# Kernel optimization log

Measured on AMD Instinct MI355X. Metric: run time of the kernel, lower is better.

## Reference

```python
import jax, jax.numpy as jnp
import numpy as np

B, N = 4, 2048

def setup_inputs() -> dict:
    key = jax.random.key(0)
    k1, k2, k3, k4 = jax.random.split(key, 4)
    return {
        "xyz": jax.random.normal(k1, (B, N, 3), dtype=jnp.float32),
        "scales": jax.random.uniform(k2, (B, N, 3), dtype=jnp.float32),
        "rotations": jax.random.normal(k3, (B, N, 4), dtype=jnp.float32),
        "velocities": jax.random.normal(k4, (B, N, 3), dtype=jnp.float32),
    }

def _quat_to_rotmat(q):
    # q: (B, N, 4) -> (B, N, 3, 3), same formula as the torch module (no normalization)
    qw, qx, qy, qz = q[..., 0], q[..., 1], q[..., 2], q[..., 3]
    R = jnp.stack([
        1 - 2 * qy**2 - 2 * qz**2, 2 * qx * qy - 2 * qz * qw, 2 * qx * qz + 2 * qy * qw,
        2 * qx * qy + 2 * qz * qw, 1 - 2 * qx**2 - 2 * qz**2, 2 * qy * qz - 2 * qx * qw,
        2 * qx * qz - 2 * qy * qw, 2 * qy * qz + 2 * qx * qw, 1 - 2 * qx**2 - 2 * qy**2,
    ], axis=-1)
    return R.reshape(q.shape[0], q.shape[1], 3, 3)

def reference(xyz, scales, rotations, velocities):
    b, n, _ = xyz.shape
    diff = xyz[:, :, None, :] - xyz[:, None, :, :]          # (B,N,N,3)
    dist = jnp.sqrt(jnp.sum(diff * diff, axis=-1) + 1e-8)    # (B,N,N)
    direction = diff / dist[..., None]                        # (B,N,N,3)

    R = _quat_to_rotmat(rotations)                            # (B,N,3,3)
    u_R = jnp.einsum('bnmi,bnij->bnmj', direction, R)         # (B,N,N,3)
    u_R_S = u_R * scales[:, None, :, :]                       # scale of gaussian m
    r_directional = jnp.sqrt(jnp.sum(u_R_S * u_R_S, axis=-1))  # (B,N,N)
    r_total = r_directional + jnp.swapaxes(r_directional, 1, 2)

    overlap = jax.nn.relu(r_total - dist)                     # (B,N,N)
    spectral_repulsion = overlap**2 / (1 + 0.1 * overlap)

    v_rel = velocities[:, :, None, :] - velocities[:, None, :, :]
    v_approach = jnp.sum(v_rel * direction, axis=-1)          # (B,N,N)
    mskd_loss = jnp.sum(overlap * jax.nn.relu(-v_approach)) / (b * n * n)

    mask = jnp.eye(n, dtype=bool)[None]                       # zero self-pairs
    spectral_repulsion = jnp.where(mask, 0.0, spectral_repulsion)
    return jnp.mean(spectral_repulsion) + 0.1 * mskd_loss
```

## Files before the change

kernel.cpp:

```cpp
#include <hip/hip_runtime.h>

#define BB 4
#define NN 2048
#define NPTS (BB * NN)
#define TILE 512
#define TT (NN / TILE)
#define NTP (TT * (TT + 1) / 2)
#define MS 32
#define MSPL (TILE / MS)
#define JPB (NTP * MSPL)
#define NJOBS (JPB * BB)
#define BLK 256
#define ROWS 2
#define SCALE (2.0f / ((float)BB * (float)NN * (float)NN))

#define WS_COUNTER_OFF 0
#define WS_PART_OFF    256
#define WS_PACK_OFF    (1 << 20)
#define WS_NEEDED      (WS_PACK_OFF + (size_t)NPTS * 5 * 16)

__device__ __forceinline__ void quat_to_R(float qw, float qx, float qy, float qz, float* R) {
    R[0] = 1.f - 2.f * (qy * qy + qz * qz);
    R[1] = 2.f * (qx * qy - qz * qw);
    R[2] = 2.f * (qx * qz + qy * qw);
    R[3] = 2.f * (qx * qy + qz * qw);
    R[4] = 1.f - 2.f * (qx * qx + qz * qz);
    R[5] = 2.f * (qy * qz - qx * qw);
    R[6] = 2.f * (qx * qz - qy * qw);
    R[7] = 2.f * (qy * qz + qx * qw);
    R[8] = 1.f - 2.f * (qx * qx + qy * qy);
}

__global__ __launch_bounds__(256) void pack_kernel(
    const float* __restrict__ xyz, const float* __restrict__ scales,
    const float* __restrict__ rot, const float* __restrict__ vel,
    float4* __restrict__ pk)
{
    const int i = blockIdx.x * 256 + threadIdx.x;
    if (i >= NPTS) return;
    const size_t i3 = 3 * (size_t)i;
    const float4 q = *reinterpret_cast<const float4*>(rot + 4 * (size_t)i);
    float R[9];
    quat_to_R(q.x, q.y, q.z, q.w, R);
    pk[0 * NPTS + i] = make_float4(xyz[i3], xyz[i3 + 1], xyz[i3 + 2], scales[i3]);
    pk[1 * NPTS + i] = make_float4(scales[i3 + 1], scales[i3 + 2], vel[i3], vel[i3 + 1]);
    pk[2 * NPTS + i] = make_float4(vel[i3 + 2], R[0], R[1], R[2]);
    pk[3 * NPTS + i] = make_float4(R[3], R[4], R[5], R[6]);
    pk[4 * NPTS + i] = make_float4(R[7], R[8], 0.f, 0.f);
}

__global__ __launch_bounds__(BLK) void pair_kernel(
    const float4* __restrict__ pk,
    float* __restrict__ partials, unsigned int* __restrict__ counter,
    float* __restrict__ outp)
{
    __shared__ float4 sm[MS][5];
    __shared__ float wsum[4];
    __shared__ int lastflag;

    const int tid = threadIdx.x;
    const int jid = blockIdx.x;
    const int b   = jid / JPB;
    const int rem = jid % JPB;
    const int p   = rem / MSPL;
    const int sl  = rem % MSPL;

    int ti = 0;
    while ((ti + 1) * (ti + 2) / 2 <= p) ++ti;
    const int tj = p - ti * (ti + 1) / 2;
    const bool diag = (ti == tj);

    const int n0 = ti * TILE;
    const int m0 = tj * TILE + sl * MS;
    const int gb = b * NN;

    if (tid < MS) {
        const int gi = gb + m0 + tid;
        sm[tid][0] = pk[0 * NPTS + gi];
        sm[tid][1] = pk[1 * NPTS + gi];
        sm[tid][2] = pk[2 * NPTS + gi];
        sm[tid][3] = pk[3 * NPTS + gi];
        sm[tid][4] = pk[4 * NPTS + gi];
    }

    float px[ROWS], py[ROWS], pz[ROWS];
    float sx[ROWS], sy[ROWS], sz[ROWS];
    float vx[ROWS], vy[ROWS], vz[ROWS];
    float Rn[ROWS][9];
    int   nidx[ROWS];
    #pragma unroll
    for (int r = 0; r < ROWS; ++r) {
        const int n  = n0 + tid + 256 * r;
        nidx[r] = n;
        const int gi = gb + n;
        const float4 n0v = pk[0 * NPTS + gi];
        const float4 n1v = pk[1 * NPTS + gi];
        const float4 n2v = pk[2 * NPTS + gi];
        const float4 n3v = pk[3 * NPTS + gi];
        const float4 n4v = pk[4 * NPTS + gi];
        px[r] = n0v.x; py[r] = n0v.y; pz[r] = n0v.z;
        sx[r] = n0v.w; sy[r] = n1v.x; sz[r] = n1v.y;
        vx[r] = n1v.z; vy[r] = n1v.w; vz[r] = n2v.x;
        Rn[r][0] = n2v.y; Rn[r][1] = n2v.z; Rn[r][2] = n2v.w;
        Rn[r][3] = n3v.x; Rn[r][4] = n3v.y; Rn[r][5] = n3v.z;
        Rn[r][6] = n3v.w; Rn[r][7] = n4v.x; Rn[r][8] = n4v.y;
    }

    __syncthreads();

    float acc = 0.f;

    auto inner = [&](bool isDiag) {
        #pragma unroll 4
        for (int j = 0; j < MS; ++j) {
            const int m = m0 + j;
            const float4 c0 = sm[j][0];
            const float4 c1 = sm[j][1];
            const float4 c2 = sm[j][2];
            const float4 c3 = sm[j][3];
            const float4 c4 = sm[j][4];
            #pragma unroll
            for (int r = 0; r < ROWS; ++r) {
                const float dx = px[r] - c0.x, dy = py[r] - c0.y, dz = pz[r] - c0.z;
                const float d2 = fmaf(dx, dx, fmaf(dy, dy, fmaf(dz, dz, 1e-8f)));
                const float rinv = __builtin_amdgcn_rsqf(d2);
                const float a0 = fmaf(dx, Rn[r][0], fmaf(dy, Rn[r][3], dz * Rn[r][6])) * c0.w;
                const float a1 = fmaf(dx, Rn[r][1], fmaf(dy, Rn[r][4], dz * Rn[r][7])) * c1.x;
                const float a2 = fmaf(dx, Rn[r][2], fmaf(dy, Rn[r][5], dz * Rn[r][8])) * c1.y;
                const float qa = __builtin_amdgcn_sqrtf(fmaf(a0, a0, fmaf(a1, a1, a2 * a2)));
                const float b0 = fmaf(dx, c2.y, fmaf(dy, c3.x, dz * c3.w)) * sx[r];
                const float b1 = fmaf(dx, c2.z, fmaf(dy, c3.y, dz * c4.x)) * sy[r];
                const float b2 = fmaf(dx, c2.w, fmaf(dy, c3.z, dz * c4.y)) * sz[r];
                const float qb = __builtin_amdgcn_sqrtf(fmaf(b0, b0, fmaf(b1, b1, b2 * b2)));
                const float ww = fmaxf(qa + qb - d2, 0.f);
                const float ov = ww * rinv;
                const float rc = __builtin_amdgcn_rcpf(fmaf(0.1f, ov, 1.f));
                const float vdot = fmaf(vx[r] - c1.z, dx,
                                   fmaf(vy[r] - c1.w, dy, (vz[r] - c2.x) * dz));
                const float ramp = fmaxf(-vdot * rinv, 0.f);
                float t = ov * fmaf(ov, rc, 0.1f * ramp);
                if (isDiag && !(m < nidx[r])) t = 0.f;
                acc += t;
            }
        }
    };
    if (diag) inner(true); else inner(false);

    #pragma unroll
    for (int off = 32; off > 0; off >>= 1)
        acc += __shfl_down(acc, off, 64);
    if ((tid & 63) == 0) wsum[tid >> 6] = acc;
    __syncthreads();

    if (tid == 0) {
        partials[jid] = wsum[0] + wsum[1] + wsum[2] + wsum[3];
        __threadfence();
        const unsigned int done = atomicAdd(counter, 1u);
        lastflag = (done == (unsigned int)(NJOBS - 1));
    }
    __syncthreads();

    if (lastflag) {
        __threadfence();
        const float4* p4 = reinterpret_cast<const float4*>(partials);
        float s = 0.f;
        for (int i = tid; i < NJOBS / 4; i += BLK) {
            const float4 v = p4[i];
            s += v.x + v.y + v.z + v.w;
        }
        #pragma unroll
        for (int off = 32; off > 0; off >>= 1)
            s += __shfl_down(s, off, 64);
        if ((tid & 63) == 0) wsum[tid >> 6] = s;
        __syncthreads();
        if (tid == 0) outp[0] = (wsum[0] + wsum[1] + wsum[2] + wsum[3]) * SCALE;
    }
}

__global__ __launch_bounds__(256) void naive_kernel(
    const float* __restrict__ xyz, const float* __restrict__ scales,
    const float* __restrict__ rot, const float* __restrict__ vel,
    float* __restrict__ outp)
{
    const int g = blockIdx.x * 256 + threadIdx.x;
    const int b = g / NN, n = g % NN;
    const size_t i3 = ((size_t)b * NN + n) * 3;
    const float4 qn = *reinterpret_cast<const float4*>(rot + ((size_t)b * NN + n) * 4);
    float Rn[9];
    quat_to_R(qn.x, qn.y, qn.z, qn.w, Rn);
    const float px = xyz[i3], py = xyz[i3+1], pz = xyz[i3+2];
    const float sx = scales[i3], sy = scales[i3+1], sz = scales[i3+2];
    const float vx = vel[i3], vy = vel[i3+1], vz = vel[i3+2];
    float acc = 0.f;
    for (int m = 0; m < n; ++m) {
        const size_t j3 = ((size_t)b * NN + m) * 3;
        const float4 qm = *reinterpret_cast<const float4*>(rot + ((size_t)b * NN + m) * 4);
        float Rm[9];
        quat_to_R(qm.x, qm.y, qm.z, qm.w, Rm);
        const float dx = px - xyz[j3], dy = py - xyz[j3+1], dz = pz - xyz[j3+2];
        const float d2 = fmaf(dx, dx, fmaf(dy, dy, fmaf(dz, dz, 1e-8f)));
        const float rinv = __builtin_amdgcn_rsqf(d2);
        const float a0 = fmaf(dx, Rn[0], fmaf(dy, Rn[3], dz*Rn[6])) * scales[j3];
        const float a1 = fmaf(dx, Rn[1], fmaf(dy, Rn[4], dz*Rn[7])) * scales[j3+1];
        const float a2 = fmaf(dx, Rn[2], fmaf(dy, Rn[5], dz*Rn[8])) * scales[j3+2];
        const float qa = __builtin_amdgcn_sqrtf(fmaf(a0,a0,fmaf(a1,a1,a2*a2)));
        const float b0 = fmaf(dx, Rm[0], fmaf(dy, Rm[3], dz*Rm[6])) * sx;
        const float b1 = fmaf(dx, Rm[1], fmaf(dy, Rm[4], dz*Rm[7])) * sy;
        const float b2 = fmaf(dx, Rm[2], fmaf(dy, Rm[5], dz*Rm[8])) * sz;
        const float qb = __builtin_amdgcn_sqrtf(fmaf(b0,b0,fmaf(b1,b1,b2*b2)));
        const float ww = fmaxf(qa + qb - d2, 0.f);
        const float ov = ww * rinv;
        const float rc = __builtin_amdgcn_rcpf(fmaf(0.1f, ov, 1.f));
        const float vdot = fmaf(vx - vel[j3], dx, fmaf(vy - vel[j3+1], dy, (vz - vel[j3+2]) * dz));
        const float ramp = fmaxf(-vdot * rinv, 0.f);
        acc += ov * fmaf(ov, rc, 0.1f * ramp);
    }
    #pragma unroll
    for (int off = 32; off > 0; off >>= 1)
        acc += __shfl_down(acc, off, 64);
    if ((threadIdx.x & 63) == 0) atomicAdd(outp, acc * SCALE);
}

extern "C" void kernel_launch(void* const* d_in, const int* in_sizes, int n_in,
                              void* d_out, int out_size, void* d_ws, size_t ws_size,
                              hipStream_t stream)
{
    const float* xyz    = (const float*)d_in[0];
    const float* scales = (const float*)d_in[1];
    const float* rot    = (const float*)d_in[2];
    const float* vel    = (const float*)d_in[3];
    float* out = (float*)d_out;

    if (ws_size >= WS_NEEDED) {
        unsigned int* counter = (unsigned int*)((char*)d_ws + WS_COUNTER_OFF);
        float* partials       = (float*)((char*)d_ws + WS_PART_OFF);
        float4* pk            = (float4*)((char*)d_ws + WS_PACK_OFF);
        hipMemsetAsync(counter, 0, sizeof(unsigned int), stream);
        pack_kernel<<<(NPTS + 255) / 256, 256, 0, stream>>>(xyz, scales, rot, vel, pk);
        pair_kernel<<<NJOBS, BLK, 0, stream>>>(pk, partials, counter, out);
    } else {
        hipMemsetAsync(d_out, 0, sizeof(float), stream);
        naive_kernel<<<NPTS / 256, 256, 0, stream>>>(xyz, scales, rot, vel, out);
    }
}
```

Before: 37.85 us.

## Retile pair kernel to 128-row tiles with float2 packed math across warps

Shrinks the row tile from 512 to 128 and gives each warp its own 16-column slice of a 64-column chunk, while every lane handles two rows at once. The per-pair arithmetic is written with float2 vectors so the compiler can emit packed FP32 FMA/mul instructions. This produces many more, smaller blocks, which improves load balance over the triangular tile set, and the packed math cuts the number of issued VALU instructions. In exchange there are more partials to reduce and more per-block setup and staging loads per pair computed.

```diff
diff --git a/kernel.cpp b/kernel.cpp
--- a/kernel.cpp
+++ b/kernel.cpp
@@ -3,21 +3,26 @@
 #define BB 4
 #define NN 2048
 #define NPTS (BB * NN)
-#define TILE 512
-#define TT (NN / TILE)
+#define TS 128
+#define TT (NN / TS)
 #define NTP (TT * (TT + 1) / 2)
-#define MS 32
-#define MSPL (TILE / MS)
+#define MC 64
+#define MSPL (TS / MC)
+#define MPW (MC / 4)
 #define JPB (NTP * MSPL)
 #define NJOBS (JPB * BB)
 #define BLK 256
-#define ROWS 2
 #define SCALE (2.0f / ((float)BB * (float)NN * (float)NN))
 
 #define WS_COUNTER_OFF 0
 #define WS_PART_OFF    256
 #define WS_PACK_OFF    (1 << 20)
 #define WS_NEEDED      (WS_PACK_OFF + (size_t)NPTS * 5 * 16)
+
+typedef float f2 __attribute__((ext_vector_type(2)));
+
+__device__ __forceinline__ f2 ffma(f2 a, f2 b, f2 c) { return __builtin_elementwise_fma(a, b, c); }
+__device__ __forceinline__ f2 fmax2(f2 a, f2 b)      { return __builtin_elementwise_max(a, b); }
 
 __device__ __forceinline__ void quat_to_R(float qw, float qx, float qy, float qz, float* R) {
     R[0] = 1.f - 2.f * (qy * qy + qz * qz);
@@ -54,45 +59,45 @@
     float* __restrict__ partials, unsigned int* __restrict__ counter,
     float* __restrict__ outp)
 {
-    __shared__ float4 sm[MS][5];
+    __shared__ float4 sm[MC][5];
     __shared__ float wsum[4];
     __shared__ int lastflag;
 
-    const int tid = threadIdx.x;
-    const int jid = blockIdx.x;
-    const int b   = jid / JPB;
-    const int rem = jid % JPB;
-    const int p   = rem / MSPL;
-    const int sl  = rem % MSPL;
+    const int tid  = threadIdx.x;
+    const int lane = tid & 63;
+    const int w    = tid >> 6;
+    const int jid  = blockIdx.x;
+    const int b    = jid / JPB;
+    const int rem  = jid % JPB;
+    const int p    = rem / MSPL;
+    const int mcch = rem % MSPL;
 
     int ti = 0;
     while ((ti + 1) * (ti + 2) / 2 <= p) ++ti;
     const int tj = p - ti * (ti + 1) / 2;
     const bool diag = (ti == tj);
 
-    const int n0 = ti * TILE;
-    const int m0 = tj * TILE + sl * MS;
-    const int gb = b * NN;
-
-    if (tid < MS) {
-        const int gi = gb + m0 + tid;
-        sm[tid][0] = pk[0 * NPTS + gi];
-        sm[tid][1] = pk[1 * NPTS + gi];
-        sm[tid][2] = pk[2 * NPTS + gi];
-        sm[tid][3] = pk[3 * NPTS + gi];
-        sm[tid][4] = pk[4 * NPTS + gi];
-    }
-
-    float px[ROWS], py[ROWS], pz[ROWS];
-    float sx[ROWS], sy[ROWS], sz[ROWS];
-    float vx[ROWS], vy[ROWS], vz[ROWS];
-    float Rn[ROWS][9];
-    int   nidx[ROWS];
+    const int n_base = ti * TS;
+    const int m_blk  = tj * TS + mcch * MC;
+    const int gb     = b * NN;
+
+    {
+        int idx = tid;
+        #pragma unroll 2
+        for (int itr = 0; itr < 2 && idx < MC * 5; ++itr, idx += 256) {
+            const int c = idx >> 6;
+            const int j = idx & 63;
+            sm[j][c] = pk[c * NPTS + gb + m_blk + j];
+        }
+    }
+
+    const int nx = n_base + lane;
+    const int ny = nx + 64;
+    f2 px, py, pz, sx, sy, sz, vx, vy, vz;
+    f2 Rn[9];
     #pragma unroll
-    for (int r = 0; r < ROWS; ++r) {
-        const int n  = n0 + tid + 256 * r;
-        nidx[r] = n;
-        const int gi = gb + n;
+    for (int r = 0; r < 2; ++r) {
+        const int gi = gb + (r == 0 ? nx : ny);
         const float4 n0v = pk[0 * NPTS + gi];
         const float4 n1v = pk[1 * NPTS + gi];
         const float4 n2v = pk[2 * NPTS + gi];
@@ -101,55 +106,77 @@
         px[r] = n0v.x; py[r] = n0v.y; pz[r] = n0v.z;
         sx[r] = n0v.w; sy[r] = n1v.x; sz[r] = n1v.y;
         vx[r] = n1v.z; vy[r] = n1v.w; vz[r] = n2v.x;
-        Rn[r][0] = n2v.y; Rn[r][1] = n2v.z; Rn[r][2] = n2v.w;
-        Rn[r][3] = n3v.x; Rn[r][4] = n3v.y; Rn[r][5] = n3v.z;
-        Rn[r][6] = n3v.w; Rn[r][7] = n4v.x; Rn[r][8] = n4v.y;
+        Rn[0][r] = n2v.y; Rn[1][r] = n2v.z; Rn[2][r] = n2v.w;
+        Rn[3][r] = n3v.x; Rn[4][r] = n3v.y; Rn[5][r] = n3v.z;
+        Rn[6][r] = n3v.w; Rn[7][r] = n4v.x; Rn[8][r] = n4v.y;
     }
 
     __syncthreads();
 
-    float acc = 0.f;
+    f2 acc = (f2)(0.f);
+    const int jb = w * MPW;
 
     auto inner = [&](bool isDiag) {
         #pragma unroll 4
-        for (int j = 0; j < MS; ++j) {
-            const int m = m0 + j;
+        for (int jj = 0; jj < MPW; ++jj) {
+            const int j = jb + jj;
+            const int m = m_blk + j;
             const float4 c0 = sm[j][0];
             const float4 c1 = sm[j][1];
             const float4 c2 = sm[j][2];
             const float4 c3 = sm[j][3];
             const float4 c4 = sm[j][4];
-            #pragma unroll
-            for (int r = 0; r < ROWS; ++r) {
-                const float dx = px[r] - c0.x, dy = py[r] - c0.y, dz = pz[r] - c0.z;
-                const float d2 = fmaf(dx, dx, fmaf(dy, dy, fmaf(dz, dz, 1e-8f)));
-                const float rinv = __builtin_amdgcn_rsqf(d2);
-                const float a0 = fmaf(dx, Rn[r][0], fmaf(dy, Rn[r][3], dz * Rn[r][6])) * c0.w;
-                const float a1 = fmaf(dx, Rn[r][1], fmaf(dy, Rn[r][4], dz * Rn[r][7])) * c1.x;
-                const float a2 = fmaf(dx, Rn[r][2], fmaf(dy, Rn[r][5], dz * Rn[r][8])) * c1.y;
-                const float qa = __builtin_amdgcn_sqrtf(fmaf(a0, a0, fmaf(a1, a1, a2 * a2)));
-                const float b0 = fmaf(dx, c2.y, fmaf(dy, c3.x, dz * c3.w)) * sx[r];
-                const float b1 = fmaf(dx, c2.z, fmaf(dy, c3.y, dz * c4.x)) * sy[r];
-                const float b2 = fmaf(dx, c2.w, fmaf(dy, c3.z, dz * c4.y)) * sz[r];
-                const float qb = __builtin_amdgcn_sqrtf(fmaf(b0, b0, fmaf(b1, b1, b2 * b2)));
-                const float ww = fmaxf(qa + qb - d2, 0.f);
-                const float ov = ww * rinv;
-                const float rc = __builtin_amdgcn_rcpf(fmaf(0.1f, ov, 1.f));
-                const float vdot = fmaf(vx[r] - c1.z, dx,
-                                   fmaf(vy[r] - c1.w, dy, (vz[r] - c2.x) * dz));
-                const float ramp = fmaxf(-vdot * rinv, 0.f);
-                float t = ov * fmaf(ov, rc, 0.1f * ramp);
-                if (isDiag && !(m < nidx[r])) t = 0.f;
-                acc += t;
+
+            const f2 dx = px - c0.x, dy = py - c0.y, dz = pz - c0.z;
+            f2 d2 = ffma(dz, dz, (f2)(1e-8f));
+            d2 = ffma(dy, dy, d2);
+            d2 = ffma(dx, dx, d2);
+            f2 rinv;
+            rinv[0] = __builtin_amdgcn_rsqf(d2[0]);
+            rinv[1] = __builtin_amdgcn_rsqf(d2[1]);
+
+            const f2 a0 = ffma(dx, Rn[0], ffma(dy, Rn[3], dz * Rn[6])) * c0.w;
+            const f2 a1 = ffma(dx, Rn[1], ffma(dy, Rn[4], dz * Rn[7])) * c1.x;
+            const f2 a2 = ffma(dx, Rn[2], ffma(dy, Rn[5], dz * Rn[8])) * c1.y;
+            const f2 qa2 = ffma(a0, a0, ffma(a1, a1, a2 * a2));
+            f2 qa;
+            qa[0] = __builtin_amdgcn_sqrtf(qa2[0]);
+            qa[1] = __builtin_amdgcn_sqrtf(qa2[1]);
+
+            const f2 b0 = ffma(dx, (f2)(c2.y), ffma(dy, (f2)(c3.x), dz * c3.w)) * sx;
+            const f2 b1 = ffma(dx, (f2)(c2.z), ffma(dy, (f2)(c3.y), dz * c4.x)) * sy;
+            const f2 b2 = ffma(dx, (f2)(c2.w), ffma(dy, (f2)(c3.z), dz * c4.y)) * sz;
+            const f2 qb2 = ffma(b0, b0, ffma(b1, b1, b2 * b2));
+            f2 qb;
+            qb[0] = __builtin_amdgcn_sqrtf(qb2[0]);
+            qb[1] = __builtin_amdgcn_sqrtf(qb2[1]);
+
+            const f2 ww = fmax2(qa + qb - d2, (f2)(0.f));
+            const f2 ov = ww * rinv;
+            const f2 den = ffma(ov, (f2)(0.1f), (f2)(1.f));
+            f2 rc;
+            rc[0] = __builtin_amdgcn_rcpf(den[0]);
+            rc[1] = __builtin_amdgcn_rcpf(den[1]);
+
+            const f2 vdot = ffma(vx - c1.z, dx, ffma(vy - c1.w, dy, (vz - c2.x) * dz));
+            const f2 ramp = fmax2(-vdot * rinv, (f2)(0.f));
+
+            f2 t = ov * ffma(ov, rc, ramp * 0.1f);
+            if (isDiag) {
+                t[0] = (m < nx) ? t[0] : 0.f;
+                t[1] = (m < ny) ? t[1] : 0.f;
             }
+            acc += t;
         }
     };
     if (diag) inner(true); else inner(false);
 
+    float a = acc[0] + acc[1];
+
     #pragma unroll
     for (int off = 32; off > 0; off >>= 1)
-        acc += __shfl_down(acc, off, 64);
-    if ((tid & 63) == 0) wsum[tid >> 6] = acc;
+        a += __shfl_down(a, off, 64);
+    if (lane == 0) wsum[w] = a;
     __syncthreads();
 
     if (tid == 0) {
@@ -171,7 +198,7 @@
         #pragma unroll
         for (int off = 32; off > 0; off >>= 1)
             s += __shfl_down(s, off, 64);
-        if ((tid & 63) == 0) wsum[tid >> 6] = s;
+        if (lane == 0) wsum[w] = s;
         __syncthreads();
         if (tid == 0) outp[0] = (wsum[0] + wsum[1] + wsum[2] + wsum[3]) * SCALE;
     }
```

Measured after the change: 38.77 us. 2.4% more time.

## Retile pair kernel into 256-row groups with 64-column strips to trim diagonal waste

Applied to the files above, without the earlier changes.

Replaces the 512x512 triangular tile pairs (each split into 32-column slices, two rows per thread) with 256-row groups. Each group is paired only with the 64-column strips up to and including its diagonal, giving 144 jobs per batch. This is meant to cut the redundant work on diagonal tiles, which were fully computed and then masked, and it drops the tile-index search loop. Each thread now handles one row, so there is less instruction-level parallelism per thread and fewer blocks are launched. Shared memory moves to a component-major layout and is filled cooperatively by all threads.

```diff
diff --git a/kernel.cpp b/kernel.cpp
--- a/kernel.cpp
+++ b/kernel.cpp
@@ -3,15 +3,12 @@
 #define BB 4
 #define NN 2048
 #define NPTS (BB * NN)
-#define TILE 512
-#define TT (NN / TILE)
-#define NTP (TT * (TT + 1) / 2)
-#define MS 32
-#define MSPL (TILE / MS)
-#define JPB (NTP * MSPL)
+#define RGR 256
+#define NG (NN / RGR)
+#define MW 64
+#define JPB 144
 #define NJOBS (JPB * BB)
 #define BLK 256
-#define ROWS 2
 #define SCALE (2.0f / ((float)BB * (float)NN * (float)NN))
 
 #define WS_COUNTER_OFF 0
@@ -54,97 +51,77 @@
     float* __restrict__ partials, unsigned int* __restrict__ counter,
     float* __restrict__ outp)
 {
-    __shared__ float4 sm[MS][5];
+    __shared__ float4 sm[5][MW];
     __shared__ float wsum[4];
     __shared__ int lastflag;
 
     const int tid = threadIdx.x;
     const int jid = blockIdx.x;
     const int b   = jid / JPB;
-    const int rem = jid % JPB;
-    const int p   = rem / MSPL;
-    const int sl  = rem % MSPL;
-
-    int ti = 0;
-    while ((ti + 1) * (ti + 2) / 2 <= p) ++ti;
-    const int tj = p - ti * (ti + 1) / 2;
-    const bool diag = (ti == tj);
-
-    const int n0 = ti * TILE;
-    const int m0 = tj * TILE + sl * MS;
+    const int r   = jid % JPB;
+
+    int g = 0;
+    #pragma unroll
+    for (int gg = 1; gg < NG; ++gg)
+        if (r >= 2 * gg * (gg + 1)) g = gg;
+    const int s  = r - 2 * g * (g + 1);
+    const int m0 = s * MW;
+    const int n  = g * RGR + tid;
     const int gb = b * NN;
 
-    if (tid < MS) {
-        const int gi = gb + m0 + tid;
-        sm[tid][0] = pk[0 * NPTS + gi];
-        sm[tid][1] = pk[1 * NPTS + gi];
-        sm[tid][2] = pk[2 * NPTS + gi];
-        sm[tid][3] = pk[3 * NPTS + gi];
-        sm[tid][4] = pk[4 * NPTS + gi];
-    }
-
-    float px[ROWS], py[ROWS], pz[ROWS];
-    float sx[ROWS], sy[ROWS], sz[ROWS];
-    float vx[ROWS], vy[ROWS], vz[ROWS];
-    float Rn[ROWS][9];
-    int   nidx[ROWS];
-    #pragma unroll
-    for (int r = 0; r < ROWS; ++r) {
-        const int n  = n0 + tid + 256 * r;
-        nidx[r] = n;
-        const int gi = gb + n;
-        const float4 n0v = pk[0 * NPTS + gi];
-        const float4 n1v = pk[1 * NPTS + gi];
-        const float4 n2v = pk[2 * NPTS + gi];
-        const float4 n3v = pk[3 * NPTS + gi];
-        const float4 n4v = pk[4 * NPTS + gi];
-        px[r] = n0v.x; py[r] = n0v.y; pz[r] = n0v.z;
-        sx[r] = n0v.w; sy[r] = n1v.x; sz[r] = n1v.y;
-        vx[r] = n1v.z; vy[r] = n1v.w; vz[r] = n2v.x;
-        Rn[r][0] = n2v.y; Rn[r][1] = n2v.z; Rn[r][2] = n2v.w;
-        Rn[r][3] = n3v.x; Rn[r][4] = n3v.y; Rn[r][5] = n3v.z;
-        Rn[r][6] = n3v.w; Rn[r][7] = n4v.x; Rn[r][8] = n4v.y;
-    }
+    {
+        int e = tid;
+        #pragma unroll 2
+        for (int it = 0; it < 2 && e < 5 * MW; ++it, e += BLK) {
+            const int c  = e >> 6;
+            const int pt = e & 63;
+            sm[c][pt] = pk[c * NPTS + gb + m0 + pt];
+        }
+    }
+
+    const int gi = gb + n;
+    const float4 n0v = pk[0 * NPTS + gi];
+    const float4 n1v = pk[1 * NPTS + gi];
+    const float4 n2v = pk[2 * NPTS + gi];
+    const float4 n3v = pk[3 * NPTS + gi];
+    const float4 n4v = pk[4 * NPTS + gi];
+    const float px = n0v.x, py = n0v.y, pz = n0v.z;
+    const float sx = n0v.w, sy = n1v.x, sz = n1v.y;
+    const float vx = n1v.z, vy = n1v.w, vz = n2v.x;
+    const float Rn0 = n2v.y, Rn1 = n2v.z, Rn2 = n2v.w;
+    const float Rn3 = n3v.x, Rn4 = n3v.y, Rn5 = n3v.z;
+    const float Rn6 = n3v.w, Rn7 = n4v.x, Rn8 = n4v.y;
 
     __syncthreads();
 
     float acc = 0.f;
 
-    auto inner = [&](bool isDiag) {
-        #pragma unroll 4
-        for (int j = 0; j < MS; ++j) {
-            const int m = m0 + j;
-            const float4 c0 = sm[j][0];
-            const float4 c1 = sm[j][1];
-            const float4 c2 = sm[j][2];
-            const float4 c3 = sm[j][3];
-            const float4 c4 = sm[j][4];
-            #pragma unroll
-            for (int r = 0; r < ROWS; ++r) {
-                const float dx = px[r] - c0.x, dy = py[r] - c0.y, dz = pz[r] - c0.z;
-                const float d2 = fmaf(dx, dx, fmaf(dy, dy, fmaf(dz, dz, 1e-8f)));
-                const float rinv = __builtin_amdgcn_rsqf(d2);
-                const float a0 = fmaf(dx, Rn[r][0], fmaf(dy, Rn[r][3], dz * Rn[r][6])) * c0.w;
-                const float a1 = fmaf(dx, Rn[r][1], fmaf(dy, Rn[r][4], dz * Rn[r][7])) * c1.x;
-                const float a2 = fmaf(dx, Rn[r][2], fmaf(dy, Rn[r][5], dz * Rn[r][8])) * c1.y;
-                const float qa = __builtin_amdgcn_sqrtf(fmaf(a0, a0, fmaf(a1, a1, a2 * a2)));
-                const float b0 = fmaf(dx, c2.y, fmaf(dy, c3.x, dz * c3.w)) * sx[r];
-                const float b1 = fmaf(dx, c2.z, fmaf(dy, c3.y, dz * c4.x)) * sy[r];
-                const float b2 = fmaf(dx, c2.w, fmaf(dy, c3.z, dz * c4.y)) * sz[r];
-                const float qb = __builtin_amdgcn_sqrtf(fmaf(b0, b0, fmaf(b1, b1, b2 * b2)));
-                const float ww = fmaxf(qa + qb - d2, 0.f);
-                const float ov = ww * rinv;
-                const float rc = __builtin_amdgcn_rcpf(fmaf(0.1f, ov, 1.f));
-                const float vdot = fmaf(vx[r] - c1.z, dx,
-                                   fmaf(vy[r] - c1.w, dy, (vz[r] - c2.x) * dz));
-                const float ramp = fmaxf(-vdot * rinv, 0.f);
-                float t = ov * fmaf(ov, rc, 0.1f * ramp);
-                if (isDiag && !(m < nidx[r])) t = 0.f;
-                acc += t;
-            }
-        }
-    };
-    if (diag) inner(true); else inner(false);
+    #pragma unroll 4
+    for (int j = 0; j < MW; ++j) {
+        const float4 c0 = sm[0][j];
+        const float4 c1 = sm[1][j];
+        const float4 c2 = sm[2][j];
+        const float4 c3 = sm[3][j];
+        const float4 c4 = sm[4][j];
+        const float dx = px - c0.x, dy = py - c0.y, dz = pz - c0.z;
+        const float d2 = fmaf(dx, dx, fmaf(dy, dy, fmaf(dz, dz, 1e-8f)));
+        const float rinv = __builtin_amdgcn_rsqf(d2);
+        const float a0 = fmaf(dx, Rn0, fmaf(dy, Rn3, dz * Rn6)) * c0.w;
+        const float a1 = fmaf(dx, Rn1, fmaf(dy, Rn4, dz * Rn7)) * c1.x;
+        const float a2 = fmaf(dx, Rn2, fmaf(dy, Rn5, dz * Rn8)) * c1.y;
+        const float qa = __builtin_amdgcn_sqrtf(fmaf(a0, a0, fmaf(a1, a1, a2 * a2)));
+        const float b0 = fmaf(dx, c2.y, fmaf(dy, c3.x, dz * c3.w)) * sx;
+        const float b1 = fmaf(dx, c2.z, fmaf(dy, c3.y, dz * c4.x)) * sy;
+        const float b2 = fmaf(dx, c2.w, fmaf(dy, c3.z, dz * c4.y)) * sz;
+        const float qb = __builtin_amdgcn_sqrtf(fmaf(b0, b0, fmaf(b1, b1, b2 * b2)));
+        const float ww = fmaxf(qa + qb - d2, 0.f);
+        const float ov = ww * rinv;
+        const float rc = __builtin_amdgcn_rcpf(fmaf(0.1f, ov, 1.f));
+        const float vdot = fmaf(vx - c1.z, dx, fmaf(vy - c1.w, dy, (vz - c2.x) * dz));
+        const float ramp = fmaxf(-vdot * rinv, 0.f);
+        const float t = ov * fmaf(ov, rc, 0.1f * ramp);
+        acc += (m0 + j < n) ? t : 0.f;
+    }
 
     #pragma unroll
     for (int off = 32; off > 0; off >>= 1)
@@ -163,15 +140,15 @@
     if (lastflag) {
         __threadfence();
         const float4* p4 = reinterpret_cast<const float4*>(partials);
-        float s = 0.f;
+        float s2 = 0.f;
         for (int i = tid; i < NJOBS / 4; i += BLK) {
             const float4 v = p4[i];
-            s += v.x + v.y + v.z + v.w;
+            s2 += v.x + v.y + v.z + v.w;
         }
         #pragma unroll
         for (int off = 32; off > 0; off >>= 1)
-            s += __shfl_down(s, off, 64);
-        if ((tid & 63) == 0) wsum[tid >> 6] = s;
+            s2 += __shfl_down(s2, off, 64);
+        if ((tid & 63) == 0) wsum[tid >> 6] = s2;
         __syncthreads();
         if (tid == 0) outp[0] = (wsum[0] + wsum[1] + wsum[2] + wsum[3]) * SCALE;
     }
@@ -182,8 +159,8 @@
     const float* __restrict__ rot, const float* __restrict__ vel,
     float* __restrict__ outp)
 {
-    const int g = blockIdx.x * 256 + threadIdx.x;
-    const int b = g / NN, n = g % NN;
+    const int gth = blockIdx.x * 256 + threadIdx.x;
+    const int b = gth / NN, n = gth % NN;
     const size_t i3 = ((size_t)b * NN + n) * 3;
     const float4 qn = *reinterpret_cast<const float4*>(rot + ((size_t)b * NN + n) * 4);
     float Rn[9];
```

Measured after the change: 36.56 us. 1.04x faster.
